# Kernel optimization log

Measured on AMD Instinct MI355X. Metric: run time of the kernel, lower is better.

The kernel has to match this reference:

```python
import jax, jax.numpy as jnp
import numpy as np

D_MODEL = 1024
D_HIDDEN = 4096
NUM_EXPERT = 8
TOP_K = 2
B, N = 1, 8192


def setup_inputs() -> dict:
    key = jax.random.key(0)
    ks = jax.random.split(key, 8)
    s1 = 1.0 / np.sqrt(D_MODEL)
    s2 = 1.0 / np.sqrt(D_HIDDEN)
    return {
        "x": jax.random.normal(ks[0], (B, N, D_MODEL), jnp.float32),
        "expert_tokens": jax.random.normal(ks[1], (NUM_EXPERT, D_MODEL), jnp.float32),
        "W1": jax.random.normal(ks[2], (NUM_EXPERT, D_MODEL, D_HIDDEN), jnp.float32) * s1,
        "b1": jnp.zeros((NUM_EXPERT, D_HIDDEN), jnp.float32),
        "W2": jax.random.normal(ks[3], (NUM_EXPERT, D_HIDDEN, D_HIDDEN), jnp.float32) * s2,
        "b2": jnp.zeros((NUM_EXPERT, D_HIDDEN), jnp.float32),
        "W3": jax.random.normal(ks[4], (NUM_EXPERT, D_HIDDEN, D_MODEL), jnp.float32) * s2,
        "b3": jnp.zeros((NUM_EXPERT, D_MODEL), jnp.float32),
    }


def _expert_mlp(x, W1, b1, W2, b2, W3, b3):
    # Linear -> GELU (exact, matching torch nn.GELU) -> Linear -> GELU -> Linear
    h = jax.nn.gelu(jnp.einsum("bnd,dh->bnh", x, W1) + b1, approximate=False)
    h = jax.nn.gelu(jnp.einsum("bnh,hk->bnk", h, W2) + b2, approximate=False)
    return jnp.einsum("bnh,hd->bnd", h, W3) + b3


def reference(x, expert_tokens, W1, b1, W2, b2, W3, b3):
    # router scores: [B, N, E]
    scores = jnp.einsum("bnd,ed->bne", x, expert_tokens)
    _, topk_idx = jax.lax.top_k(scores, TOP_K)  # [B, N, TOP_K]
    outputs = jnp.zeros_like(x)
    num_expert = W1.shape[0]
    for i in range(num_expert):
        # gate weight = (# of top-k slots assigned to expert i) / top_k
        w = jnp.mean((topk_idx == i).astype(x.dtype), axis=-1, keepdims=True)
        y = _expert_mlp(x, W1[i], b1[i], W2[i], b2[i], W3[i], b3[i])
        outputs = outputs + y * w
    return outputs
```

## Files before the change

kernel.cpp:

```cpp
#include <hip/hip_runtime.h>
#include <stdint.h>

#define D_MODEL 1024
#define D_HID   4096
#define NEXP    8
#define NTOK    8192
#define TOTROW  (NTOK*2)

typedef unsigned short ushort_t;
typedef __attribute__((ext_vector_type(8))) short short8;
typedef __attribute__((ext_vector_type(4))) float f32x4;

static __device__ __forceinline__ ushort_t f2bf(float f) {
    union { float f; uint32_t u; } v; v.f = f;
    uint32_t u = v.u;
    uint32_t r = (u + 0x7FFFu + ((u >> 16) & 1u)) >> 16;
    return (ushort_t)r;
}
static __device__ __forceinline__ float bf2f(ushort_t h) {
    union { uint32_t u; float f; } v; v.u = ((uint32_t)h) << 16;
    return v.f;
}
static __device__ __forceinline__ float gelu_f(float x) {
    return 0.5f * x * (1.0f + erff(x * 0.70710678118654752f));
}

static __device__ __forceinline__ void gload_lds16(const void* g, void* l) {
    __builtin_amdgcn_global_load_lds(
        (const __attribute__((address_space(1))) void*)g,
        (__attribute__((address_space(3))) void*)l,
        16, 0, 0);
}

__global__ __launch_bounds__(256) void router_kernel(
    const float* __restrict__ x, const float* __restrict__ et,
    int* __restrict__ cnt, int* __restrict__ top2, ushort_t* __restrict__ xb)
{
    __shared__ float lds_et[NEXP * D_MODEL];
    int t = threadIdx.x;
    #pragma unroll
    for (int i = 0; i < (NEXP * D_MODEL) / 256; ++i)
        lds_et[i * 256 + t] = et[i * 256 + t];
    __syncthreads();

    int lane = t & 63, wv = t >> 6;
    int n = blockIdx.x * 4 + wv;
    double s[NEXP];
    #pragma unroll
    for (int e = 0; e < NEXP; ++e) s[e] = 0.0;
    const float* xr = x + (size_t)n * D_MODEL;
    ushort_t* xbr = xb + (size_t)n * D_MODEL;
    for (int it = 0; it < D_MODEL / 64; ++it) {
        float xv = xr[it * 64 + lane];
        xbr[it * 64 + lane] = f2bf(xv);
        #pragma unroll
        for (int e = 0; e < NEXP; ++e)
            s[e] += (double)(xv * lds_et[e * D_MODEL + it * 64 + lane]);
    }
    #pragma unroll
    for (int e = 0; e < NEXP; ++e)
        for (int off = 32; off; off >>= 1)
            s[e] += __shfl_xor(s[e], off);

    if (lane == 0) {
        int e1 = 0;
        for (int e = 1; e < NEXP; ++e) if (s[e] > s[e1]) e1 = e;
        int e2 = (e1 == 0) ? 1 : 0;
        for (int e = 0; e < NEXP; ++e) if (e != e1 && s[e] > s[e2]) e2 = e;
        top2[n * 2 + 0] = e1;
        top2[n * 2 + 1] = e2;
        atomicAdd(&cnt[e1], 1);
        atomicAdd(&cnt[e2], 1);
    }
}

__global__ void scan_kernel(const int* __restrict__ cnt, int* __restrict__ base,
                            int* __restrict__ cnt2)
{
    if (threadIdx.x == 0 && blockIdx.x == 0) {
        int acc = 0;
        for (int e = 0; e < NEXP; ++e) { base[e] = acc; acc += cnt[e]; cnt2[e] = 0; }
    }
}

__global__ __launch_bounds__(256) void assign_kernel(
    const int* __restrict__ top2, const int* __restrict__ base,
    int* __restrict__ cnt2, int* __restrict__ rowinfo, int* __restrict__ token_rows)
{
    int n = blockIdx.x * 256 + threadIdx.x;
    if (n >= NTOK) return;
    #pragma unroll
    for (int k = 0; k < 2; ++k) {
        int e = top2[n * 2 + k];
        int slot = atomicAdd(&cnt2[e], 1);
        int row = base[e] + slot;
        rowinfo[row] = n;
        token_rows[n * 2 + k] = row;
    }
}

__global__ __launch_bounds__(256) void transpose_kernel(
    const float* __restrict__ in, ushort_t* __restrict__ out, int K, int N, int ntiles)
{
    __shared__ ushort_t tile[64][132];
    const int t = threadIdx.x;
    const int m = t & 15;
    const int g = t >> 4;
    const int npt = N >> 6;
    const int tpe = (K >> 7) * npt;

    for (int tid = blockIdx.x; tid < ntiles; tid += gridDim.x) {
        int e = tid / tpe;
        int rem = tid - e * tpe;
        int ky = rem / npt;
        int nx = rem - ky * npt;
        const float* ine = in + (size_t)e * K * N + (size_t)(ky * 128) * N + nx * 64;
        ushort_t* oute = out + (size_t)e * N * K + (size_t)(nx * 64) * K + ky * 128;

        float4 f[8];
        #pragma unroll
        for (int i = 0; i < 8; ++i)
            f[i] = *(const float4*)(ine + (size_t)(g * 8 + i) * N + m * 4);
        #pragma unroll
        for (int j = 0; j < 4; ++j) {
            ushort_t o[8];
            o[0] = f2bf(f[0].x * 0 + ((const float*)&f[0])[j]);
            #pragma unroll
            for (int i = 0; i < 8; ++i) o[i] = f2bf(((const float*)&f[i])[j]);
            *(uint4*)&tile[m * 4 + j][g * 8] = *(const uint4*)o;
        }
        __syncthreads();
        #pragma unroll
        for (int p = 0; p < 4; ++p) {
            int n = p * 16 + g;
            uint4 v = *(const uint4*)&tile[n][m * 8];
            *(uint4*)(oute + (size_t)n * K + m * 8) = v;
        }
        __syncthreads();
    }
}


#define RD_A(BUF, MH) do {                                                        \
    _Pragma("unroll") for (int mi = 0; mi < 4; ++mi) {                            \
        areg[mi][0] = *(const short8*)(pA0 + (BUF)*16384 + (MH)*4096 + mi*1024);  \
        areg[mi][1] = *(const short8*)(pA1 + (BUF)*16384 + (MH)*4096 + mi*1024);  \
    }                                                                             \
} while (0)

#define RD_B(DST, BUF, NH) do {                                                   \
    _Pragma("unroll") for (int ni = 0; ni < 2; ++ni) {                            \
        DST[ni][0] = *(const short8*)(pB0 + (BUF)*16384 + (NH)*2048 + ni*1024);   \
        DST[ni][1] = *(const short8*)(pB1 + (BUF)*16384 + (NH)*2048 + ni*1024);   \
    }                                                                             \
} while (0)

#define MM(BR, MH, NH) do {                                                       \
    __builtin_amdgcn_s_setprio(1);                                                \
    _Pragma("unroll") for (int mi = 0; mi < 4; ++mi)                              \
    _Pragma("unroll") for (int ni = 0; ni < 2; ++ni)                              \
    _Pragma("unroll") for (int ks = 0; ks < 2; ++ks)                              \
      acc[(MH)*4 + mi][(NH)*2 + ni] = __builtin_amdgcn_mfma_f32_16x16x32_bf16(    \
          areg[mi][ks], BR[ni][ks], acc[(MH)*4 + mi][(NH)*2 + ni], 0, 0, 0);      \
    __builtin_amdgcn_s_setprio(0);                                                \
} while (0)

#define PH(MH, NH, BR, TAIL) do { MM(BR, MH, NH); TAIL; __builtin_amdgcn_s_barrier(); } while (0)

#define VW6 asm volatile("s_waitcnt vmcnt(6)" ::: "memory")
#define VW0 asm volatile("s_waitcnt vmcnt(0)" ::: "memory")

template<bool GATHER, bool GELU_ACT>
__global__ __launch_bounds__(512, 2) void moe_gemm8(
    const ushort_t* __restrict__ Ah,
    const ushort_t* __restrict__ BT,
    const float* __restrict__ bias,
    ushort_t* __restrict__ C,
    const int* __restrict__ cnt, const int* __restrict__ basep,
    const int* __restrict__ rowinfo,
    int Ncols, int K)
{
    const int e = blockIdx.z;
    const int cnte = cnt[e];
    const int mt = blockIdx.y;
    if (mt * 256 >= cnte) return;
    const int base_e = basep[e];
    const int row0 = base_e + mt * 256;
    const int col0 = blockIdx.x * 256;

    __shared__ __attribute__((aligned(16))) ushort_t SMEM[2][2][256][64];

    const int t = threadIdx.x;
    const int lane = t & 63;
    const int wv = t >> 6;
    const int wm = wv >> 2;
    const int wn = wv & 3;
    const int l15 = lane & 15, lhi = lane >> 4;
    const int key = l15 & 7;
    const int lr8 = lane >> 3;
    const int sl  = (lane & 7) ^ lr8;

    const int slot0 = (lhi ^ key) * 8;
    const int slot1 = ((4 + lhi) ^ key) * 8;
    const ushort_t* pA0 = &SMEM[0][0][wm * 128 + l15][slot0];
    const ushort_t* pA1 = &SMEM[0][0][wm * 128 + l15][slot1];
    const ushort_t* pB0 = &SMEM[1][0][wn * 64 + l15][slot0];
    const ushort_t* pB1 = &SMEM[1][0][wn * 64 + l15][slot1];

    uint32_t aOff[2][2], bOff[2][2];
    #pragma unroll
    for (int mh = 0; mh < 2; ++mh)
        #pragma unroll
        for (int c = 0; c < 2; ++c) {
            int tr = mh * 64 + wv * 8 + lr8 + c * 128;
            int gr = row0 + tr; if (gr > TOTROW - 1) gr = TOTROW - 1;
            uint32_t rowid = GATHER ? (uint32_t)rowinfo[gr] : (uint32_t)gr;
            aOff[mh][c] = rowid * (uint32_t)(K * 2) + sl * 16;
        }
    #pragma unroll
    for (int nh = 0; nh < 2; ++nh)
        #pragma unroll
        for (int c = 0; c < 2; ++c) {
            int tr = (wv >> 2) * 64 + nh * 32 + (wv & 3) * 8 + lr8 + c * 128;
            bOff[nh][c] = ((uint32_t)e * Ncols + col0 + tr) * (uint32_t)(K * 2) + sl * 16;
        }

    const int arb = wv * 8;
    const int brb = (wv >> 2) * 64 + (wv & 3) * 8;

    auto stageA = [&](int buf, int mh) {
        gload_lds16((const char*)Ah + aOff[mh][0], (void*)&SMEM[0][buf][mh * 64 + arb][0]);
        gload_lds16((const char*)Ah + aOff[mh][1], (void*)&SMEM[0][buf][128 + mh * 64 + arb][0]);
        aOff[mh][0] += 128; aOff[mh][1] += 128;
    };
    auto stageB = [&](int buf, int nh) {
        gload_lds16((const char*)BT + bOff[nh][0], (void*)&SMEM[1][buf][nh * 32 + brb][0]);
        gload_lds16((const char*)BT + bOff[nh][1], (void*)&SMEM[1][buf][128 + nh * 32 + brb][0]);
        bOff[nh][0] += 128; bOff[nh][1] += 128;
    };

    f32x4 acc[8][4];
    #pragma unroll
    for (int i = 0; i < 8; ++i)
        #pragma unroll
        for (int j = 0; j < 4; ++j)
            acc[i][j] = (f32x4){0.f, 0.f, 0.f, 0.f};

    short8 areg[4][2], breg0[2][2], breg1[2][2];

    const int KT = K / 64;
    const int NIT = KT / 2;

    stageA(0, 0); stageB(0, 0); stageB(0, 1); stageA(0, 1);
    stageA(1, 0); stageB(1, 0); stageB(1, 1); stageA(1, 1);
    VW0;
    __builtin_amdgcn_s_barrier();
    RD_A(0, 0); RD_B(breg0, 0, 0);

    for (int i2 = 0; i2 < NIT - 1; ++i2) {
         PH(0, 0, breg0, { stageA(0, 0); RD_B(breg1, 0, 1); });
         PH(0, 1, breg1, { stageB(0, 0); RD_A(0, 1); });
         PH(1, 1, breg1, { stageB(0, 1); VW6; });
         PH(1, 0, breg0, { stageA(0, 1); RD_A(1, 0); RD_B(breg0, 1, 0); });
         PH(0, 0, breg0, { stageA(1, 0); RD_B(breg1, 1, 1); });
         PH(0, 1, breg1, { stageB(1, 0); RD_A(1, 1); });
         PH(1, 1, breg1, { stageB(1, 1); VW6; });
         PH(1, 0, breg0, { stageA(1, 1); RD_A(0, 0); RD_B(breg0, 0, 0); });
    }
    {
         PH(0, 0, breg0, { RD_B(breg1, 0, 1); });
         PH(0, 1, breg1, { RD_A(0, 1); });
         PH(1, 1, breg1, { VW0; });
         PH(1, 0, breg0, { RD_A(1, 0); RD_B(breg0, 1, 0); });
         PH(0, 0, breg0, { RD_B(breg1, 1, 1); });
         PH(0, 1, breg1, { RD_A(1, 1); });
         PH(1, 1, breg1, { });
         MM(breg0, 1, 0);
    }

    ushort_t* ctile = &SMEM[0][0][0][0];
    #pragma unroll
    for (int n = 0; n < 4; ++n) {
        int c = wn * 64 + n * 16 + l15;
        float bv = bias[e * Ncols + col0 + c];
        #pragma unroll
        for (int m = 0; m < 8; ++m) {
            #pragma unroll
            for (int q = 0; q < 4; ++q) {
                int r = wm * 128 + m * 16 + lhi * 4 + q;
                float v = acc[m][n][q] + bv;
                if (GELU_ACT) v = gelu_f(v);
                ctile[r * 256 + ((c >> 3) ^ ((r & 7) << 2)) * 8 + (c & 7)] = f2bf(v);
            }
        }
    }
    __syncthreads();
    {
        int rr = t >> 2;
        int ch0 = t & 3;
        #pragma unroll
        for (int pass = 0; pass < 2; ++pass) {
            int r = pass * 128 + rr;
            int rl = mt * 256 + r;
            if (rl < cnte) {
                size_t gbase = (size_t)(base_e + rl) * Ncols + col0;
                #pragma unroll
                for (int i = 0; i < 8; ++i) {
                    int ch = ch0 + i * 4;
                    uint4 v = *(const uint4*)&ctile[r * 256 + ((ch ^ ((r & 7) << 2)) * 8)];
                    *(uint4*)&C[gbase + ch * 8] = v;
                }
            }
        }
    }
}

__global__ __launch_bounds__(256) void combine_kernel(
    const ushort_t* __restrict__ Y, const int* __restrict__ token_rows,
    float* __restrict__ out)
{
    int t = threadIdx.x;
    for (int n = blockIdx.x; n < NTOK; n += gridDim.x) {
        int r1 = token_rows[n * 2 + 0], r2 = token_rows[n * 2 + 1];
        const ushort_t* y1 = Y + (size_t)r1 * D_MODEL + t * 4;
        const ushort_t* y2 = Y + (size_t)r2 * D_MODEL + t * 4;
        ushort_t a[4], b[4];
        *(uint2*)a = *(const uint2*)y1;
        *(uint2*)b = *(const uint2*)y2;
        float4 o;
        o.x = 0.5f * (bf2f(a[0]) + bf2f(b[0]));
        o.y = 0.5f * (bf2f(a[1]) + bf2f(b[1]));
        o.z = 0.5f * (bf2f(a[2]) + bf2f(b[2]));
        o.w = 0.5f * (bf2f(a[3]) + bf2f(b[3]));
        *(float4*)(out + (size_t)n * D_MODEL + t * 4) = o;
    }
}

extern "C" void kernel_launch(void* const* d_in, const int* in_sizes, int n_in,
                              void* d_out, int out_size, void* d_ws, size_t ws_size,
                              hipStream_t stream)
{
    const float* x  = (const float*)d_in[0];
    const float* et = (const float*)d_in[1];
    const float* W1 = (const float*)d_in[2];
    const float* b1 = (const float*)d_in[3];
    const float* W2 = (const float*)d_in[4];
    const float* b2 = (const float*)d_in[5];
    const float* W3 = (const float*)d_in[6];
    const float* b3 = (const float*)d_in[7];
    float* out = (float*)d_out;

    char* ws = (char*)d_ws;
    size_t off = 0;
    auto alloc = [&](size_t bytes) -> char* {
        char* p = ws + off;
        off += (bytes + 255) & ~(size_t)255;
        return p;
    };
    int* cnt        = (int*)alloc(NEXP * 4);
    int* basep      = (int*)alloc(NEXP * 4);
    int* cnt2       = (int*)alloc(NEXP * 4);
    int* top2       = (int*)alloc((size_t)NTOK * 2 * 4);
    int* token_rows = (int*)alloc((size_t)NTOK * 2 * 4);
    int* rowinfo    = (int*)alloc((size_t)TOTROW * 4);
    ushort_t* W1T = (ushort_t*)alloc((size_t)NEXP * D_HID * D_MODEL * 2);
    ushort_t* W2T = (ushort_t*)alloc((size_t)NEXP * D_HID * D_HID * 2);
    ushort_t* W3T = (ushort_t*)alloc((size_t)NEXP * D_MODEL * D_HID * 2);
    ushort_t* H1  = (ushort_t*)alloc((size_t)TOTROW * D_HID * 2);
    ushort_t* H2  = (ushort_t*)alloc((size_t)TOTROW * D_HID * 2);
    ushort_t* Yr  = (ushort_t*)alloc((size_t)TOTROW * D_MODEL * 2);
    if (off > ws_size) return;

    ushort_t* xb = H2;

    hipMemsetAsync(cnt, 0, NEXP * 4, stream);
    router_kernel<<<NTOK / 4, 256, 0, stream>>>(x, et, cnt, top2, xb);
    scan_kernel<<<1, 64, 0, stream>>>(cnt, basep, cnt2);
    assign_kernel<<<NTOK / 256, 256, 0, stream>>>(top2, basep, cnt2, rowinfo, token_rows);

    {
        int nt1 = (D_MODEL / 128) * (D_HID / 64) * NEXP;
        int nt2 = (D_HID / 128) * (D_HID / 64) * NEXP;
        int nt3 = (D_HID / 128) * (D_MODEL / 64) * NEXP;
        transpose_kernel<<<2048, 256, 0, stream>>>(W1, W1T, D_MODEL, D_HID, nt1);
        transpose_kernel<<<2048, 256, 0, stream>>>(W2, W2T, D_HID, D_HID, nt2);
        transpose_kernel<<<2048, 256, 0, stream>>>(W3, W3T, D_HID, D_MODEL, nt3);
    }

    moe_gemm8<true, true><<<dim3(D_HID / 256, 16, NEXP), 512, 0, stream>>>(
        xb, W1T, b1, H1, cnt, basep, rowinfo, D_HID, D_MODEL);
    moe_gemm8<false, true><<<dim3(D_HID / 256, 16, NEXP), 512, 0, stream>>>(
        H1, W2T, b2, H2, cnt, basep, rowinfo, D_HID, D_HID);
    moe_gemm8<false, false><<<dim3(D_MODEL / 256, 16, NEXP), 512, 0, stream>>>(
        H2, W3T, b3, Yr, cnt, basep, rowinfo, D_MODEL, D_HID);

    combine_kernel<<<2048, 256, 0, stream>>>(Yr, token_rows, out);
}
```

Measured before the change: 1.517 ms.

## Halve GEMM barriers per k-step and restructure weight transpose into column bands

The MoE GEMM main loop now places a workgroup barrier after every two MFMA phases instead of after each one. It adds sched_barrier fences around the barriers and relaxes the global-load wait to vmcnt(4), placed just before the LDS reads that depend on it. The weight transpose kernel now gives each block a whole 64-column band (optionally split along K), loops over its K tiles, and runs with fewer blocks. The aim is to cut synchronization stalls in the GEMM and improve memory locality in the transpose, at the risk of LDS hazards from the looser barrier and wait placement and of lower parallelism in the transpose.

```diff
diff --git a/kernel.cpp b/kernel.cpp
--- a/kernel.cpp
+++ b/kernel.cpp
@@ -100,43 +100,47 @@
 }
 
 __global__ __launch_bounds__(256) void transpose_kernel(
-    const float* __restrict__ in, ushort_t* __restrict__ out, int K, int N, int ntiles)
+    const float* __restrict__ in, ushort_t* __restrict__ out, int K, int N,
+    int nwork, int ksplit)
 {
     __shared__ ushort_t tile[64][132];
     const int t = threadIdx.x;
     const int m = t & 15;
     const int g = t >> 4;
-    const int npt = N >> 6;
-    const int tpe = (K >> 7) * npt;
-
-    for (int tid = blockIdx.x; tid < ntiles; tid += gridDim.x) {
-        int e = tid / tpe;
-        int rem = tid - e * tpe;
-        int ky = rem / npt;
-        int nx = rem - ky * npt;
-        const float* ine = in + (size_t)e * K * N + (size_t)(ky * 128) * N + nx * 64;
-        ushort_t* oute = out + (size_t)e * N * K + (size_t)(nx * 64) * K + ky * 128;
-
-        float4 f[8];
-        #pragma unroll
-        for (int i = 0; i < 8; ++i)
-            f[i] = *(const float4*)(ine + (size_t)(g * 8 + i) * N + m * 4);
-        #pragma unroll
-        for (int j = 0; j < 4; ++j) {
-            ushort_t o[8];
-            o[0] = f2bf(f[0].x * 0 + ((const float*)&f[0])[j]);
+    const int bpe = N >> 6;
+    const int kyt = (K >> 7) / ksplit;
+
+    for (int wid = blockIdx.x; wid < nwork; wid += gridDim.x) {
+        int band = wid / ksplit;
+        int kc = wid - band * ksplit;
+        int e = band / bpe, nx = band - e * bpe;
+        const float* ine0 = in + (size_t)e * K * N + nx * 64 + (size_t)(kc * kyt * 128) * N;
+        ushort_t* oute0 = out + (size_t)e * N * K + (size_t)(nx * 64) * K + kc * kyt * 128;
+
+        for (int ky = 0; ky < kyt; ++ky) {
+            const float* ine = ine0 + (size_t)(ky * 128) * N;
+            ushort_t* oute = oute0 + ky * 128;
+
+            float4 f[8];
             #pragma unroll
-            for (int i = 0; i < 8; ++i) o[i] = f2bf(((const float*)&f[i])[j]);
-            *(uint4*)&tile[m * 4 + j][g * 8] = *(const uint4*)o;
+            for (int i = 0; i < 8; ++i)
+                f[i] = *(const float4*)(ine + (size_t)(g * 8 + i) * N + m * 4);
+            #pragma unroll
+            for (int j = 0; j < 4; ++j) {
+                ushort_t o[8];
+                #pragma unroll
+                for (int i = 0; i < 8; ++i) o[i] = f2bf(((const float*)&f[i])[j]);
+                *(uint4*)&tile[m * 4 + j][g * 8] = *(const uint4*)o;
+            }
+            __syncthreads();
+            #pragma unroll
+            for (int p = 0; p < 4; ++p) {
+                int n = p * 16 + g;
+                uint4 v = *(const uint4*)&tile[n][m * 8];
+                *(uint4*)(oute + (size_t)n * K + m * 8) = v;
+            }
+            __syncthreads();
         }
-        __syncthreads();
-        #pragma unroll
-        for (int p = 0; p < 4; ++p) {
-            int n = p * 16 + g;
-            uint4 v = *(const uint4*)&tile[n][m * 8];
-            *(uint4*)(oute + (size_t)n * K + m * 8) = v;
-        }
-        __syncthreads();
     }
 }
 
@@ -165,10 +169,10 @@
     __builtin_amdgcn_s_setprio(0);                                                \
 } while (0)
 
-#define PH(MH, NH, BR, TAIL) do { MM(BR, MH, NH); TAIL; __builtin_amdgcn_s_barrier(); } while (0)
-
-#define VW6 asm volatile("s_waitcnt vmcnt(6)" ::: "memory")
-#define VW0 asm volatile("s_waitcnt vmcnt(0)" ::: "memory")
+#define SCH0 __builtin_amdgcn_sched_barrier(0)
+#define SBAR do { SCH0; __builtin_amdgcn_s_barrier(); SCH0; } while (0)
+#define VW4  asm volatile("s_waitcnt vmcnt(4)" ::: "memory")
+#define VW0  asm volatile("s_waitcnt vmcnt(0)" ::: "memory")
 
 template<bool GATHER, bool GELU_ACT>
 __global__ __launch_bounds__(512, 2) void moe_gemm8(
@@ -258,23 +262,23 @@
     RD_A(0, 0); RD_B(breg0, 0, 0);
 
     for (int i2 = 0; i2 < NIT - 1; ++i2) {
-         PH(0, 0, breg0, { stageA(0, 0); RD_B(breg1, 0, 1); });
-         PH(0, 1, breg1, { stageB(0, 0); RD_A(0, 1); });
-         PH(1, 1, breg1, { stageB(0, 1); VW6; });
-         PH(1, 0, breg0, { stageA(0, 1); RD_A(1, 0); RD_B(breg0, 1, 0); });
-         PH(0, 0, breg0, { stageA(1, 0); RD_B(breg1, 1, 1); });
-         PH(0, 1, breg1, { stageB(1, 0); RD_A(1, 1); });
-         PH(1, 1, breg1, { stageB(1, 1); VW6; });
-         PH(1, 0, breg0, { stageA(1, 1); RD_A(0, 0); RD_B(breg0, 0, 0); });
+         MM(breg0, 0, 0); stageA(0, 0); RD_B(breg1, 0, 1);
+         MM(breg1, 0, 1); stageB(0, 0); RD_A(0, 1);                       SBAR;
+         MM(breg1, 1, 1); stageB(0, 1);
+         MM(breg0, 1, 0); stageA(0, 1); VW4; RD_A(1, 0); RD_B(breg0, 1, 0); SBAR;
+         MM(breg0, 0, 0); stageA(1, 0); RD_B(breg1, 1, 1);
+         MM(breg1, 0, 1); stageB(1, 0); RD_A(1, 1);                       SBAR;
+         MM(breg1, 1, 1); stageB(1, 1);
+         MM(breg0, 1, 0); stageA(1, 1); VW4; RD_A(0, 0); RD_B(breg0, 0, 0); SBAR;
     }
     {
-         PH(0, 0, breg0, { RD_B(breg1, 0, 1); });
-         PH(0, 1, breg1, { RD_A(0, 1); });
-         PH(1, 1, breg1, { VW0; });
-         PH(1, 0, breg0, { RD_A(1, 0); RD_B(breg0, 1, 0); });
-         PH(0, 0, breg0, { RD_B(breg1, 1, 1); });
-         PH(0, 1, breg1, { RD_A(1, 1); });
-         PH(1, 1, breg1, { });
+         MM(breg0, 0, 0); RD_B(breg1, 0, 1);
+         MM(breg1, 0, 1); RD_A(0, 1); VW0;                                 SBAR;
+         MM(breg1, 1, 1);
+         MM(breg0, 1, 0); RD_A(1, 0); RD_B(breg0, 1, 0);
+         MM(breg0, 0, 0); RD_B(breg1, 1, 1);
+         MM(breg1, 0, 1); RD_A(1, 1);                                      SBAR;
+         MM(breg1, 1, 1);
          MM(breg0, 1, 0);
     }
 
@@ -379,12 +383,12 @@
     assign_kernel<<<NTOK / 256, 256, 0, stream>>>(top2, basep, cnt2, rowinfo, token_rows);
 
     {
-        int nt1 = (D_MODEL / 128) * (D_HID / 64) * NEXP;
-        int nt2 = (D_HID / 128) * (D_HID / 64) * NEXP;
-        int nt3 = (D_HID / 128) * (D_MODEL / 64) * NEXP;
-        transpose_kernel<<<2048, 256, 0, stream>>>(W1, W1T, D_MODEL, D_HID, nt1);
-        transpose_kernel<<<2048, 256, 0, stream>>>(W2, W2T, D_HID, D_HID, nt2);
-        transpose_kernel<<<2048, 256, 0, stream>>>(W3, W3T, D_HID, D_MODEL, nt3);
+        int nb1 = (D_HID / 64) * NEXP;
+        int nb2 = (D_HID / 64) * NEXP;
+        int nb3 = (D_MODEL / 64) * NEXP;
+        transpose_kernel<<<512, 256, 0, stream>>>(W1, W1T, D_MODEL, D_HID, nb1, 1);
+        transpose_kernel<<<512, 256, 0, stream>>>(W2, W2T, D_HID, D_HID, nb2, 1);
+        transpose_kernel<<<256, 256, 0, stream>>>(W3, W3T, D_HID, D_MODEL, nb3 * 2, 2);
     }
 
     moe_gemm8<true, true><<<dim3(D_HID / 256, 16, NEXP), 512, 0, stream>>>(
```

Result: slower. 1.551 ms (+2.2%).
